# Kernel optimization log

Measured on AMD Instinct MI355X. Metric: run time of the kernel, lower is better.

## Reference

```python
import jax, jax.numpy as jnp
import numpy as np

EMBEDDING_DIM = 768
ATTENTION_HEADS = 12
N = 1024
BATCH = 8
D_HEAD = EMBEDDING_DIM // ATTENTION_HEADS  # 64


def setup_inputs() -> dict:
    key = jax.random.key(0)
    ks = jax.random.split(key, 6)
    return {
        "embeddings": jax.random.normal(ks[0], (BATCH, N, EMBEDDING_DIM), dtype=jnp.float32),
        "B_matrix": jax.random.normal(ks[1], (1, ATTENTION_HEADS, N, N), dtype=jnp.float32),
        "WQ": jax.random.normal(ks[2], (EMBEDDING_DIM, EMBEDDING_DIM), dtype=jnp.float32),
        "WK": jax.random.normal(ks[3], (EMBEDDING_DIM, EMBEDDING_DIM), dtype=jnp.float32),
        "WV": jax.random.normal(ks[4], (EMBEDDING_DIM, EMBEDDING_DIM), dtype=jnp.float32),
        "WO": jax.random.normal(ks[5], (EMBEDDING_DIM, EMBEDDING_DIM), dtype=jnp.float32),
    }


def reference(embeddings, B_matrix, WQ, WK, WV, WO):
    H, d = ATTENTION_HEADS, D_HEAD
    scale = 1.0 / jnp.sqrt(jnp.float32(d))
    # Faithful to original: reshape(-1, H, N, d) directly (NOT a head-split transpose).
    Qh = (embeddings @ WQ).reshape(-1, H, N, d)   # [B, H, N, d]
    Kh = (embeddings @ WK).reshape(-1, H, N, d)
    Vh = (embeddings @ WV).reshape(-1, H, N, d)
    scores = jnp.einsum("bhnd,bhmd->bhnm", Qh, Kh) * scale  # [B, H, N, N]
    attn = jax.nn.softmax(scores + B_matrix, axis=-1)
    Hc = jnp.einsum("bhnm,bhmd->bhnd", attn, Vh)  # [B, H, N, d]
    Hc = Hc.transpose(0, 2, 1, 3).reshape(-1, N, EMBEDDING_DIM)  # [B, N, E]
    return Hc @ WO
```

## Files before the change

### kernel.cpp

```cpp
#include <hip/hip_runtime.h>
#include <math.h>

#define EDIM 768
#define NSEQ 1024
#define NB 8
#define NH 12
#define DH 64

typedef __attribute__((ext_vector_type(8))) short bh8;
typedef __attribute__((ext_vector_type(4))) float f4;
typedef __attribute__((ext_vector_type(8))) unsigned short us8;
typedef __attribute__((ext_vector_type(4))) unsigned short us4;

#define MFMA(a, b, c) __builtin_amdgcn_mfma_f32_16x16x32_bf16((bh8)(a), (bh8)(b), (c), 0, 0, 0)

__device__ __forceinline__ unsigned short f2bf(float x) {
    union { float f; unsigned u; } v; v.f = x;
    unsigned r = v.u + 0x7fff + ((v.u >> 16) & 1);
    return (unsigned short)(r >> 16);
}
__device__ __forceinline__ float bf2f(unsigned short b) {
    union { float f; unsigned u; } v; v.u = ((unsigned)b) << 16;
    return v.f;
}

template <int C>
__device__ __forceinline__ float dppmov(float x) {
    union { int i; float f; } u; u.f = x;
    u.i = __builtin_amdgcn_update_dpp(0, u.i, C, 0xF, 0xF, true);
    return u.f;
}
__device__ __forceinline__ float rowmax16(float x) {
    x = fmaxf(x, dppmov<0x121>(x));
    x = fmaxf(x, dppmov<0x122>(x));
    x = fmaxf(x, dppmov<0x124>(x));
    x = fmaxf(x, dppmov<0x128>(x));
    return x;
}
__device__ __forceinline__ float rowsum16(float x) {
    x += dppmov<0x121>(x);
    x += dppmov<0x122>(x);
    x += dppmov<0x124>(x);
    x += dppmov<0x128>(x);
    return x;
}

__global__ __launch_bounds__(256)
void conv_emb(const float* __restrict__ E, unsigned short* __restrict__ Eh,
              unsigned short* __restrict__ El)
{
    size_t idx = ((size_t)blockIdx.x * 256 + threadIdx.x) * 4;
    float4 v = *(const float4*)&E[idx];
    us4 h, l;
    h.x = f2bf(v.x); l.x = f2bf(v.x - bf2f(h.x));
    h.y = f2bf(v.y); l.y = f2bf(v.y - bf2f(h.y));
    h.z = f2bf(v.z); l.z = f2bf(v.z - bf2f(h.z));
    h.w = f2bf(v.w); l.w = f2bf(v.w - bf2f(h.w));
    *(us4*)&Eh[idx] = h;
    *(us4*)&El[idx] = l;
}

__global__ __launch_bounds__(256)
void conv_w(const float* __restrict__ W0, const float* __restrict__ W1,
            const float* __restrict__ W2, const float* __restrict__ W3,
            unsigned short* __restrict__ Wbase)
{
    const int z = blockIdx.z;
    const float* __restrict__ W = (z == 0) ? W0 : (z == 1) ? W1 : (z == 2) ? W2 : W3;
    unsigned short* __restrict__ Wh = Wbase + (size_t)z * 2 * (EDIM * EDIM);
    unsigned short* __restrict__ Wl = Wh + (EDIM * EDIM);

    __shared__ float T[64][65];
    const int t = threadIdx.x;
    const int n0 = blockIdx.x * 64, k0 = blockIdx.y * 64;

#pragma unroll
    for (int rr = 0; rr < 4; rr++) {
        int row = rr * 16 + (t >> 4);
        int c4  = (t & 15) * 4;
        float4 v = *(const float4*)&W[(size_t)(k0 + row) * EDIM + n0 + c4];
        T[row][c4 + 0] = v.x; T[row][c4 + 1] = v.y;
        T[row][c4 + 2] = v.z; T[row][c4 + 3] = v.w;
    }
    __syncthreads();
#pragma unroll
    for (int rr = 0; rr < 4; rr++) {
        int nn = rr * 16 + (t >> 4);
        int k4 = (t & 15) * 4;
        us4 h, l;
        float v0 = T[k4 + 0][nn], v1 = T[k4 + 1][nn],
              v2 = T[k4 + 2][nn], v3 = T[k4 + 3][nn];
        h.x = f2bf(v0); l.x = f2bf(v0 - bf2f(h.x));
        h.y = f2bf(v1); l.y = f2bf(v1 - bf2f(h.y));
        h.z = f2bf(v2); l.z = f2bf(v2 - bf2f(h.z));
        h.w = f2bf(v3); l.w = f2bf(v3 - bf2f(h.w));
        size_t o = (size_t)(n0 + nn) * EDIM + k0 + k4;
        *(us4*)&Wh[o] = h;
        *(us4*)&Wl[o] = l;
    }
}

__global__ __launch_bounds__(256)
void qkv_gemm(const unsigned short* __restrict__ Eh, const unsigned short* __restrict__ El,
              const unsigned short* __restrict__ Wbase,
              unsigned short* __restrict__ Qh, unsigned short* __restrict__ Ql,
              unsigned short* __restrict__ Kh, unsigned short* __restrict__ Kl,
              unsigned short* __restrict__ Vt)
{
    const int bid = blockIdx.x;
    const int xcd = bid & 7, j = bid >> 3;
    const int mblk = xcd * 8 + (j / 18);
    const int rest = j % 18;
    const int nblk = rest % 6, z = rest / 6;

    const unsigned short* __restrict__ Wh = Wbase + (size_t)z * 2 * (EDIM * EDIM);
    const unsigned short* __restrict__ Wl = Wh + (EDIM * EDIM);

    __shared__ unsigned short Ahq[4][128][8], Alq[4][128][8];
    __shared__ unsigned short Bhq[4][128][8], Blq[4][128][8];

    const int t = threadIdx.x;
    const int wave = t >> 6, lane = t & 63;
    const int quad = lane >> 4, l16 = lane & 15;
    const int wm = (wave >> 1) * 64, wn = (wave & 1) * 64;
    const int m0 = mblk * 128, n0 = nblk * 128;

    const int sr = t >> 1, q0 = (t & 1) * 2;

    f4 acc[4][4];
#pragma unroll
    for (int i = 0; i < 4; i++)
#pragma unroll
        for (int j2 = 0; j2 < 4; j2++) acc[i][j2] = (f4){0.f, 0.f, 0.f, 0.f};

    const size_t abase = (size_t)(m0 + sr) * EDIM + q0 * 8;
    const size_t bbase = (size_t)(n0 + sr) * EDIM + q0 * 8;

    us8 a0 = *(const us8*)&Eh[abase], a1 = *(const us8*)&Eh[abase + 8];
    us8 b0 = *(const us8*)&Wh[bbase], b1 = *(const us8*)&Wh[bbase + 8];
    us8 a2, a3, b2, b3;
    if (z != 2) {
        a2 = *(const us8*)&El[abase]; a3 = *(const us8*)&El[abase + 8];
        b2 = *(const us8*)&Wl[bbase]; b3 = *(const us8*)&Wl[bbase + 8];
    }

    for (int it = 0; it < 24; it++) {
        __syncthreads();
        *(us8*)&Ahq[q0][sr][0] = a0; *(us8*)&Ahq[q0 + 1][sr][0] = a1;
        *(us8*)&Bhq[q0][sr][0] = b0; *(us8*)&Bhq[q0 + 1][sr][0] = b1;
        if (z != 2) {
            *(us8*)&Alq[q0][sr][0] = a2; *(us8*)&Alq[q0 + 1][sr][0] = a3;
            *(us8*)&Blq[q0][sr][0] = b2; *(us8*)&Blq[q0 + 1][sr][0] = b3;
        }
        __syncthreads();

        {
            const int kn = (it < 23) ? (it + 1) * 32 : 0;
            a0 = *(const us8*)&Eh[abase + kn]; a1 = *(const us8*)&Eh[abase + kn + 8];
            b0 = *(const us8*)&Wh[bbase + kn]; b1 = *(const us8*)&Wh[bbase + kn + 8];
            if (z != 2) {
                a2 = *(const us8*)&El[abase + kn]; a3 = *(const us8*)&El[abase + kn + 8];
                b2 = *(const us8*)&Wl[bbase + kn]; b3 = *(const us8*)&Wl[bbase + kn + 8];
            }
        }

        bh8 aH[4], bH[4];
#pragma unroll
        for (int mt = 0; mt < 4; mt++)
            aH[mt] = *(const bh8*)&Ahq[quad][wm + mt * 16 + l16][0];
#pragma unroll
        for (int nt = 0; nt < 4; nt++)
            bH[nt] = *(const bh8*)&Bhq[quad][wn + nt * 16 + l16][0];

        if (z != 2) {
            bh8 aL[4], bL[4];
#pragma unroll
            for (int mt = 0; mt < 4; mt++)
                aL[mt] = *(const bh8*)&Alq[quad][wm + mt * 16 + l16][0];
#pragma unroll
            for (int nt = 0; nt < 4; nt++)
                bL[nt] = *(const bh8*)&Blq[quad][wn + nt * 16 + l16][0];
#pragma unroll
            for (int mt = 0; mt < 4; mt++)
#pragma unroll
                for (int nt = 0; nt < 4; nt++) {
                    acc[mt][nt] = MFMA(aH[mt], bH[nt], acc[mt][nt]);
                    acc[mt][nt] = MFMA(aH[mt], bL[nt], acc[mt][nt]);
                    acc[mt][nt] = MFMA(aL[mt], bH[nt], acc[mt][nt]);
                }
        } else {
#pragma unroll
            for (int mt = 0; mt < 4; mt++)
#pragma unroll
                for (int nt = 0; nt < 4; nt++)
                    acc[mt][nt] = MFMA(aH[mt], bH[nt], acc[mt][nt]);
        }
    }

#pragma unroll
    for (int mt = 0; mt < 4; mt++)
#pragma unroll
        for (int nt = 0; nt < 4; nt++)
#pragma unroll
            for (int r = 0; r < 4; r++) {
                int row = m0 + wm + mt * 16 + quad * 4 + r;
                int col = n0 + wn + nt * 16 + l16;
                float v = acc[mt][nt][r];
                if (z == 2) {
                    int bb = row >> 10, nr = row & 1023;
                    int g = nr * 12 + (col >> 6);
                    int hh = g >> 10, key = g & 1023, dim = col & 63;
                    Vt[(((size_t)(bb * NH + hh)) * DH + dim) * NSEQ + key] = f2bf(v);
                } else {
                    unsigned short h = f2bf(v);
                    unsigned short l = f2bf(v - bf2f(h));
                    size_t o = (size_t)row * EDIM + col;
                    if (z == 0) { Qh[o] = h; Ql[o] = l; }
                    else        { Kh[o] = h; Kl[o] = l; }
                }
            }
}

__global__ __launch_bounds__(256)
void attn_mfma(const unsigned short* __restrict__ Qh, const unsigned short* __restrict__ Ql,
               const unsigned short* __restrict__ Kh, const unsigned short* __restrict__ Kl,
               const unsigned short* __restrict__ Vt, const float* __restrict__ Bm,
               unsigned short* __restrict__ Hc)
{
    const int bid = blockIdx.x;
    const int xcd = bid & 7, j = bid >> 3;
    const int combo = xcd * 12 + (j >> 4);
    const int rt = j & 15;
    const int h = combo >> 3, b = combo & 7;
    const int r0 = rt * 64;

    __shared__ unsigned short Khs[64][72], Kls[64][72];
    __shared__ unsigned short Vts[64][72];
    __shared__ unsigned short Ps[4][16][68];

    const int t = threadIdx.x;
    const int wave = t >> 6, lane = t & 63;
    const int quad = lane >> 4, l16 = lane & 15;
    const int wr = wave * 16;

    const int srow = t >> 2, sseg = (t & 3) * 16;

    const size_t hb = (size_t)b * (NSEQ * EDIM) + (size_t)h * (NSEQ * DH);
    const size_t vb = (((size_t)(b * NH + h)) * DH) * NSEQ;

    const size_t kbase = hb + (size_t)srow * DH + sseg;
    const size_t vbase = vb + (size_t)srow * NSEQ + sseg;

    bh8 qfh[2], qfl[2];
    {
        const size_t qo = hb + (size_t)(r0 + srow) * DH + sseg;
        us8 q0 = *(const us8*)&Qh[qo], q1 = *(const us8*)&Qh[qo + 8];
        us8 q2 = *(const us8*)&Ql[qo], q3 = *(const us8*)&Ql[qo + 8];
        *(us8*)&Khs[srow][sseg] = q0; *(us8*)&Khs[srow][sseg + 8] = q1;
        *(us8*)&Kls[srow][sseg] = q2; *(us8*)&Kls[srow][sseg + 8] = q3;
        __syncthreads();
#pragma unroll
        for (int ks = 0; ks < 2; ks++) {
            qfh[ks] = *(const bh8*)&Khs[wr + l16][ks * 32 + quad * 8];
            qfl[ks] = *(const bh8*)&Kls[wr + l16][ks * 32 + quad * 8];
        }
    }

    us8 k0v = *(const us8*)&Kh[kbase],     k1v = *(const us8*)&Kh[kbase + 8];
    us8 k2v = *(const us8*)&Kl[kbase],     k3v = *(const us8*)&Kl[kbase + 8];
    us8 v0v = *(const us8*)&Vt[vbase],     v1v = *(const us8*)&Vt[vbase + 8];

    float m[4] = {-3e38f, -3e38f, -3e38f, -3e38f};
    float lsum[4] = {0.f, 0.f, 0.f, 0.f};
    f4 o[4];
#pragma unroll
    for (int dt = 0; dt < 4; dt++) o[dt] = (f4){0.f, 0.f, 0.f, 0.f};

    const float* bb = Bm + ((size_t)h << 20) + ((size_t)(r0 + wr + quad * 4) << 10) + l16;

    for (int kt = 0; kt < 16; kt++) {
        const int c0 = kt * 64;
        __syncthreads();
        *(us8*)&Khs[srow][sseg] = k0v; *(us8*)&Khs[srow][sseg + 8] = k1v;
        *(us8*)&Kls[srow][sseg] = k2v; *(us8*)&Kls[srow][sseg + 8] = k3v;
        *(us8*)&Vts[srow][sseg] = v0v; *(us8*)&Vts[srow][sseg + 8] = v1v;
        __syncthreads();

        {
            const int cn = ((kt + 1) & 15) * 64;
            k0v = *(const us8*)&Kh[kbase + (size_t)cn * DH];
            k1v = *(const us8*)&Kh[kbase + (size_t)cn * DH + 8];
            k2v = *(const us8*)&Kl[kbase + (size_t)cn * DH];
            k3v = *(const us8*)&Kl[kbase + (size_t)cn * DH + 8];
            v0v = *(const us8*)&Vt[vbase + cn];
            v1v = *(const us8*)&Vt[vbase + cn + 8];
        }

        float bv[4][4];
#pragma unroll
        for (int ct = 0; ct < 4; ct++)
#pragma unroll
            for (int r = 0; r < 4; r++)
                bv[ct][r] = bb[(size_t)r * NSEQ + c0 + ct * 16];

        f4 s[4];
#pragma unroll
        for (int ct = 0; ct < 4; ct++) {
            bh8 kh0 = *(const bh8*)&Khs[ct * 16 + l16][quad * 8];
            bh8 kh1 = *(const bh8*)&Khs[ct * 16 + l16][32 + quad * 8];
            bh8 kl0 = *(const bh8*)&Kls[ct * 16 + l16][quad * 8];
            bh8 kl1 = *(const bh8*)&Kls[ct * 16 + l16][32 + quad * 8];
            f4 a = (f4){0.f, 0.f, 0.f, 0.f};
            a = MFMA(qfh[0], kh0, a); a = MFMA(qfh[1], kh1, a);
            a = MFMA(qfl[0], kh0, a); a = MFMA(qfl[1], kh1, a);
            a = MFMA(qfh[0], kl0, a); a = MFMA(qfh[1], kl1, a);
            s[ct] = a;
        }
#pragma unroll
        for (int ct = 0; ct < 4; ct++)
#pragma unroll
            for (int r = 0; r < 4; r++)
                s[ct][r] = fmaf(s[ct][r], 0.125f, bv[ct][r]);

        float alpha[4];
#pragma unroll
        for (int r = 0; r < 4; r++) {
            float mx = fmaxf(fmaxf(s[0][r], s[1][r]), fmaxf(s[2][r], s[3][r]));
            mx = rowmax16(mx);
            float mn = fmaxf(m[r], mx);
            alpha[r] = __expf(m[r] - mn);
            m[r] = mn;
        }
#pragma unroll
        for (int ct = 0; ct < 4; ct++)
#pragma unroll
            for (int r = 0; r < 4; r++)
                s[ct][r] = __expf(s[ct][r] - m[r]);
#pragma unroll
        for (int r = 0; r < 4; r++) {
            float ls = rowsum16(s[0][r] + s[1][r] + s[2][r] + s[3][r]);
            lsum[r] = lsum[r] * alpha[r] + ls;
        }
#pragma unroll
        for (int dt = 0; dt < 4; dt++)
#pragma unroll
            for (int r = 0; r < 4; r++) o[dt][r] *= alpha[r];

#pragma unroll
        for (int ct = 0; ct < 4; ct++)
#pragma unroll
            for (int r = 0; r < 4; r++)
                Ps[wave][quad * 4 + r][ct * 16 + l16] = f2bf(s[ct][r]);

        bh8 p0 = *(const bh8*)&Ps[wave][l16][quad * 8];
        bh8 p1 = *(const bh8*)&Ps[wave][l16][32 + quad * 8];
#pragma unroll
        for (int dt = 0; dt < 4; dt++) {
            bh8 v0 = *(const bh8*)&Vts[dt * 16 + l16][quad * 8];
            bh8 v1 = *(const bh8*)&Vts[dt * 16 + l16][32 + quad * 8];
            o[dt] = MFMA(p0, v0, o[dt]);
            o[dt] = MFMA(p1, v1, o[dt]);
        }
    }

#pragma unroll
    for (int r = 0; r < 4; r++) lsum[r] = 1.f / lsum[r];
#pragma unroll
    for (int dt = 0; dt < 4; dt++)
#pragma unroll
        for (int r = 0; r < 4; r++) {
            int row = r0 + wr + quad * 4 + r;
            int col = h * DH + dt * 16 + l16;
            Hc[(size_t)(b * NSEQ + row) * EDIM + col] = f2bf(o[dt][r] * lsum[r]);
        }
}

__global__ __launch_bounds__(256)
void out_gemm(const unsigned short* __restrict__ A, const unsigned short* __restrict__ Wh,
              float* __restrict__ C)
{
    const int bid = blockIdx.x;
    const int xcd = bid & 7, j = bid >> 3;
    const int mblk = xcd * 8 + (j / 6);
    const int nblk = j % 6;

    __shared__ unsigned short Ahq[4][128][8];
    __shared__ unsigned short Bhq[4][128][8];

    const int t = threadIdx.x;
    const int wave = t >> 6, lane = t & 63;
    const int quad = lane >> 4, l16 = lane & 15;
    const int wm = (wave >> 1) * 64, wn = (wave & 1) * 64;
    const int m0 = mblk * 128, n0 = nblk * 128;
    const int sr = t >> 1, q0 = (t & 1) * 2;

    f4 acc[4][4];
#pragma unroll
    for (int i = 0; i < 4; i++)
#pragma unroll
        for (int j2 = 0; j2 < 4; j2++) acc[i][j2] = (f4){0.f, 0.f, 0.f, 0.f};

    const size_t abase = (size_t)(m0 + sr) * EDIM + q0 * 8;
    const size_t bbase = (size_t)(n0 + sr) * EDIM + q0 * 8;

    us8 a0 = *(const us8*)&A[abase],  a1 = *(const us8*)&A[abase + 8];
    us8 b0 = *(const us8*)&Wh[bbase], b1 = *(const us8*)&Wh[bbase + 8];

    for (int it = 0; it < 24; it++) {
        __syncthreads();
        *(us8*)&Ahq[q0][sr][0] = a0; *(us8*)&Ahq[q0 + 1][sr][0] = a1;
        *(us8*)&Bhq[q0][sr][0] = b0; *(us8*)&Bhq[q0 + 1][sr][0] = b1;
        __syncthreads();

        {
            const int kn = (it < 23) ? (it + 1) * 32 : 0;
            a0 = *(const us8*)&A[abase + kn];  a1 = *(const us8*)&A[abase + kn + 8];
            b0 = *(const us8*)&Wh[bbase + kn]; b1 = *(const us8*)&Wh[bbase + kn + 8];
        }

        bh8 aF[4], bF[4];
#pragma unroll
        for (int mt = 0; mt < 4; mt++)
            aF[mt] = *(const bh8*)&Ahq[quad][wm + mt * 16 + l16][0];
#pragma unroll
        for (int nt = 0; nt < 4; nt++)
            bF[nt] = *(const bh8*)&Bhq[quad][wn + nt * 16 + l16][0];
#pragma unroll
        for (int mt = 0; mt < 4; mt++)
#pragma unroll
            for (int nt = 0; nt < 4; nt++)
                acc[mt][nt] = MFMA(aF[mt], bF[nt], acc[mt][nt]);
    }

#pragma unroll
    for (int mt = 0; mt < 4; mt++)
#pragma unroll
        for (int nt = 0; nt < 4; nt++)
#pragma unroll
            for (int r = 0; r < 4; r++) {
                int row = m0 + wm + mt * 16 + quad * 4 + r;
                int col = n0 + wn + nt * 16 + l16;
                C[(size_t)row * EDIM + col] = acc[mt][nt][r];
            }
}

extern "C" void kernel_launch(void* const* d_in, const int* in_sizes, int n_in,
                              void* d_out, int out_size, void* d_ws, size_t ws_size,
                              hipStream_t stream)
{
    const float* emb = (const float*)d_in[0];
    const float* Bm  = (const float*)d_in[1];
    const float* WQ  = (const float*)d_in[2];
    const float* WK  = (const float*)d_in[3];
    const float* WV  = (const float*)d_in[4];
    const float* WO  = (const float*)d_in[5];
    float* out = (float*)d_out;

    const size_t SZ = (size_t)NB * NSEQ * EDIM;
    const size_t WSZ = (size_t)EDIM * EDIM;

    unsigned short* p  = (unsigned short*)d_ws;
    unsigned short* Eh = p;                  p += SZ;
    unsigned short* El = p;                  p += SZ;
    unsigned short* Wb = p;                  p += 8 * WSZ;
    unsigned short* Qh = p;                  p += SZ;
    unsigned short* Ql = p;                  p += SZ;
    unsigned short* Kh = p;                  p += SZ;
    unsigned short* Kl = p;                  p += SZ;
    unsigned short* Vt = p;                  p += SZ;
    unsigned short* Hc = Eh;

    conv_emb<<<dim3(SZ / (256 * 4)), dim3(256), 0, stream>>>(emb, Eh, El);
    conv_w<<<dim3(EDIM / 64, EDIM / 64, 4), dim3(256), 0, stream>>>(WQ, WK, WV, WO, Wb);

    qkv_gemm<<<dim3(1152), dim3(256), 0, stream>>>(
        Eh, El, Wb, Qh, Ql, Kh, Kl, Vt);

    attn_mfma<<<dim3(1536), dim3(256), 0, stream>>>(
        Qh, Ql, Kh, Kl, Vt, Bm, Hc);

    out_gemm<<<dim3(384), dim3(256), 0, stream>>>(
        Hc, Wb + 6 * WSZ, out);
}
```

Before: 337.4 us.

## Use direct global-to-LDS loads with XOR-swizzled layout in QKV and output GEMMs

Replaces the register-staged global loads and LDS stores in the QKV and output projection GEMMs with global_load_lds 16-byte direct transfers into a flat, XOR-swizzled LDS layout. Fragment reads use matching swizzled offsets to avoid bank conflicts. This removes register staging and VGPR pressure. It also drops the software prefetch of the next K tile, so load latency is no longer overlapped with MFMA work inside a block and depends on occupancy instead.

```diff
diff --git a/kernel.cpp b/kernel.cpp
--- a/kernel.cpp
+++ b/kernel.cpp
@@ -22,6 +22,12 @@
 __device__ __forceinline__ float bf2f(unsigned short b) {
     union { float f; unsigned u; } v; v.u = ((unsigned)b) << 16;
     return v.f;
+}
+
+__device__ __forceinline__ void gl2lds16(const unsigned short* g, unsigned short* l) {
+    __builtin_amdgcn_global_load_lds(
+        (const __attribute__((address_space(1))) unsigned int*)g,
+        (__attribute__((address_space(3))) unsigned int*)l, 16, 0, 0);
 }
 
 template <int C>
@@ -116,8 +122,8 @@
     const unsigned short* __restrict__ Wh = Wbase + (size_t)z * 2 * (EDIM * EDIM);
     const unsigned short* __restrict__ Wl = Wh + (EDIM * EDIM);
 
-    __shared__ unsigned short Ahq[4][128][8], Alq[4][128][8];
-    __shared__ unsigned short Bhq[4][128][8], Blq[4][128][8];
+    __shared__ unsigned short Ahq[4096], Alq[4096];
+    __shared__ unsigned short Bhq[4096], Blq[4096];
 
     const int t = threadIdx.x;
     const int wave = t >> 6, lane = t & 63;
@@ -125,7 +131,22 @@
     const int wm = (wave >> 1) * 64, wn = (wave & 1) * 64;
     const int m0 = mblk * 128, n0 = nblk * 128;
 
-    const int sr = t >> 1, q0 = (t & 1) * 2;
+    const int s0 = wave * 128 + lane, s1 = s0 + 64;
+    const int r0s = s0 >> 2, q0s = (s0 & 3) ^ ((r0s >> 1) & 3);
+    const int r1s = s1 >> 2, q1s = (s1 & 3) ^ ((r1s >> 1) & 3);
+    size_t ga0 = (size_t)(m0 + r0s) * EDIM + q0s * 8;
+    size_t ga1 = (size_t)(m0 + r1s) * EDIM + q1s * 8;
+    size_t gb0 = (size_t)(n0 + r0s) * EDIM + q0s * 8;
+    size_t gb1 = (size_t)(n0 + r1s) * EDIM + q1s * 8;
+    const int d0 = (wave * 128) * 8, d1 = (wave * 128 + 64) * 8;
+
+    const int qp = quad ^ ((l16 >> 1) & 3);
+    int offA[4], offB[4];
+#pragma unroll
+    for (int i = 0; i < 4; i++) {
+        offA[i] = (wm + i * 16 + l16) * 32 + qp * 8;
+        offB[i] = (wn + i * 16 + l16) * 32 + qp * 8;
+    }
 
     f4 acc[4][4];
 #pragma unroll
@@ -133,53 +154,28 @@
 #pragma unroll
         for (int j2 = 0; j2 < 4; j2++) acc[i][j2] = (f4){0.f, 0.f, 0.f, 0.f};
 
-    const size_t abase = (size_t)(m0 + sr) * EDIM + q0 * 8;
-    const size_t bbase = (size_t)(n0 + sr) * EDIM + q0 * 8;
-
-    us8 a0 = *(const us8*)&Eh[abase], a1 = *(const us8*)&Eh[abase + 8];
-    us8 b0 = *(const us8*)&Wh[bbase], b1 = *(const us8*)&Wh[bbase + 8];
-    us8 a2, a3, b2, b3;
-    if (z != 2) {
-        a2 = *(const us8*)&El[abase]; a3 = *(const us8*)&El[abase + 8];
-        b2 = *(const us8*)&Wl[bbase]; b3 = *(const us8*)&Wl[bbase + 8];
-    }
-
     for (int it = 0; it < 24; it++) {
-        __syncthreads();
-        *(us8*)&Ahq[q0][sr][0] = a0; *(us8*)&Ahq[q0 + 1][sr][0] = a1;
-        *(us8*)&Bhq[q0][sr][0] = b0; *(us8*)&Bhq[q0 + 1][sr][0] = b1;
+        gl2lds16(&Eh[ga0], &Ahq[d0]); gl2lds16(&Eh[ga1], &Ahq[d1]);
+        gl2lds16(&Wh[gb0], &Bhq[d0]); gl2lds16(&Wh[gb1], &Bhq[d1]);
         if (z != 2) {
-            *(us8*)&Alq[q0][sr][0] = a2; *(us8*)&Alq[q0 + 1][sr][0] = a3;
-            *(us8*)&Blq[q0][sr][0] = b2; *(us8*)&Blq[q0 + 1][sr][0] = b3;
-        }
-        __syncthreads();
-
-        {
-            const int kn = (it < 23) ? (it + 1) * 32 : 0;
-            a0 = *(const us8*)&Eh[abase + kn]; a1 = *(const us8*)&Eh[abase + kn + 8];
-            b0 = *(const us8*)&Wh[bbase + kn]; b1 = *(const us8*)&Wh[bbase + kn + 8];
-            if (z != 2) {
-                a2 = *(const us8*)&El[abase + kn]; a3 = *(const us8*)&El[abase + kn + 8];
-                b2 = *(const us8*)&Wl[bbase + kn]; b3 = *(const us8*)&Wl[bbase + kn + 8];
-            }
-        }
+            gl2lds16(&El[ga0], &Alq[d0]); gl2lds16(&El[ga1], &Alq[d1]);
+            gl2lds16(&Wl[gb0], &Blq[d0]); gl2lds16(&Wl[gb1], &Blq[d1]);
+        }
+        ga0 += 32; ga1 += 32; gb0 += 32; gb1 += 32;
+        __syncthreads();
 
         bh8 aH[4], bH[4];
 #pragma unroll
-        for (int mt = 0; mt < 4; mt++)
-            aH[mt] = *(const bh8*)&Ahq[quad][wm + mt * 16 + l16][0];
-#pragma unroll
-        for (int nt = 0; nt < 4; nt++)
-            bH[nt] = *(const bh8*)&Bhq[quad][wn + nt * 16 + l16][0];
+        for (int mt = 0; mt < 4; mt++) aH[mt] = *(const bh8*)&Ahq[offA[mt]];
+#pragma unroll
+        for (int nt = 0; nt < 4; nt++) bH[nt] = *(const bh8*)&Bhq[offB[nt]];
 
         if (z != 2) {
             bh8 aL[4], bL[4];
 #pragma unroll
-            for (int mt = 0; mt < 4; mt++)
-                aL[mt] = *(const bh8*)&Alq[quad][wm + mt * 16 + l16][0];
-#pragma unroll
-            for (int nt = 0; nt < 4; nt++)
-                bL[nt] = *(const bh8*)&Blq[quad][wn + nt * 16 + l16][0];
+            for (int mt = 0; mt < 4; mt++) aL[mt] = *(const bh8*)&Alq[offA[mt]];
+#pragma unroll
+            for (int nt = 0; nt < 4; nt++) bL[nt] = *(const bh8*)&Blq[offB[nt]];
 #pragma unroll
             for (int mt = 0; mt < 4; mt++)
 #pragma unroll
@@ -195,6 +191,7 @@
                 for (int nt = 0; nt < 4; nt++)
                     acc[mt][nt] = MFMA(aH[mt], bH[nt], acc[mt][nt]);
         }
+        __syncthreads();
     }
 
 #pragma unroll
@@ -384,15 +381,31 @@
     const int mblk = xcd * 8 + (j / 6);
     const int nblk = j % 6;
 
-    __shared__ unsigned short Ahq[4][128][8];
-    __shared__ unsigned short Bhq[4][128][8];
+    __shared__ unsigned short Ahq[4096];
+    __shared__ unsigned short Bhq[4096];
 
     const int t = threadIdx.x;
     const int wave = t >> 6, lane = t & 63;
     const int quad = lane >> 4, l16 = lane & 15;
     const int wm = (wave >> 1) * 64, wn = (wave & 1) * 64;
     const int m0 = mblk * 128, n0 = nblk * 128;
-    const int sr = t >> 1, q0 = (t & 1) * 2;
+
+    const int s0 = wave * 128 + lane, s1 = s0 + 64;
+    const int r0s = s0 >> 2, q0s = (s0 & 3) ^ ((r0s >> 1) & 3);
+    const int r1s = s1 >> 2, q1s = (s1 & 3) ^ ((r1s >> 1) & 3);
+    size_t ga0 = (size_t)(m0 + r0s) * EDIM + q0s * 8;
+    size_t ga1 = (size_t)(m0 + r1s) * EDIM + q1s * 8;
+    size_t gb0 = (size_t)(n0 + r0s) * EDIM + q0s * 8;
+    size_t gb1 = (size_t)(n0 + r1s) * EDIM + q1s * 8;
+    const int d0 = (wave * 128) * 8, d1 = (wave * 128 + 64) * 8;
+
+    const int qp = quad ^ ((l16 >> 1) & 3);
+    int offA[4], offB[4];
+#pragma unroll
+    for (int i = 0; i < 4; i++) {
+        offA[i] = (wm + i * 16 + l16) * 32 + qp * 8;
+        offB[i] = (wn + i * 16 + l16) * 32 + qp * 8;
+    }
 
     f4 acc[4][4];
 #pragma unroll
@@ -400,36 +413,23 @@
 #pragma unroll
         for (int j2 = 0; j2 < 4; j2++) acc[i][j2] = (f4){0.f, 0.f, 0.f, 0.f};
 
-    const size_t abase = (size_t)(m0 + sr) * EDIM + q0 * 8;
-    const size_t bbase = (size_t)(n0 + sr) * EDIM + q0 * 8;
-
-    us8 a0 = *(const us8*)&A[abase],  a1 = *(const us8*)&A[abase + 8];
-    us8 b0 = *(const us8*)&Wh[bbase], b1 = *(const us8*)&Wh[bbase + 8];
-
     for (int it = 0; it < 24; it++) {
-        __syncthreads();
-        *(us8*)&Ahq[q0][sr][0] = a0; *(us8*)&Ahq[q0 + 1][sr][0] = a1;
-        *(us8*)&Bhq[q0][sr][0] = b0; *(us8*)&Bhq[q0 + 1][sr][0] = b1;
-        __syncthreads();
-
-        {
-            const int kn = (it < 23) ? (it + 1) * 32 : 0;
-            a0 = *(const us8*)&A[abase + kn];  a1 = *(const us8*)&A[abase + kn + 8];
-            b0 = *(const us8*)&Wh[bbase + kn]; b1 = *(const us8*)&Wh[bbase + kn + 8];
-        }
+        gl2lds16(&A[ga0],  &Ahq[d0]); gl2lds16(&A[ga1],  &Ahq[d1]);
+        gl2lds16(&Wh[gb0], &Bhq[d0]); gl2lds16(&Wh[gb1], &Bhq[d1]);
+        ga0 += 32; ga1 += 32; gb0 += 32; gb1 += 32;
+        __syncthreads();
 
         bh8 aF[4], bF[4];
 #pragma unroll
-        for (int mt = 0; mt < 4; mt++)
-            aF[mt] = *(const bh8*)&Ahq[quad][wm + mt * 16 + l16][0];
-#pragma unroll
-        for (int nt = 0; nt < 4; nt++)
-            bF[nt] = *(const bh8*)&Bhq[quad][wn + nt * 16 + l16][0];
+        for (int mt = 0; mt < 4; mt++) aF[mt] = *(const bh8*)&Ahq[offA[mt]];
+#pragma unroll
+        for (int nt = 0; nt < 4; nt++) bF[nt] = *(const bh8*)&Bhq[offB[nt]];
 #pragma unroll
         for (int mt = 0; mt < 4; mt++)
 #pragma unroll
             for (int nt = 0; nt < 4; nt++)
                 acc[mt][nt] = MFMA(aF[mt], bF[nt], acc[mt][nt]);
+        __syncthreads();
     }
 
 #pragma unroll
```

After: 341.3 us. Within noise of the previous version (+1.2%).
